# Performance work log

Measured on AMD Instinct MI355X. Metric: run time of the kernel, lower is better.

The kernel has to match this reference:

```python
import jax, jax.numpy as jnp
import numpy as np

# Hyperparameters from init_kwargs
SMOOTHNESS = 0.5
RADIUS_RATIO = 0.1  # computed in original code but never used in the mask math
IMG_SIZE = 512
BATCH = 32


def _smooth_mask(h, w, smoothness):
    """Vectorized replacement of the original per-pixel double loop.

    mask[i,j] = smoothness                       if |i-ch|^2 + |j-cw|^2 <= 1
              = max(1, dist_norm / smoothness)   otherwise
    where dist_norm = sqrt((|i-ch|/(h/2))^2 + (|j-cw|/(w/2))^2).
    Returns [h, w] float32 (broadcasts over the channel dim).
    """
    dh = jnp.abs(jnp.arange(h, dtype=jnp.float32) - (h // 2))[:, None]  # [h,1]
    dw = jnp.abs(jnp.arange(w, dtype=jnp.float32) - (w // 2))[None, :]  # [1,w]
    center = dh * dh + dw * dw <= 1.0
    dist = jnp.sqrt((dh / (h / 2)) ** 2 + (dw / (w / 2)) ** 2)
    outer = jnp.maximum(jnp.float32(1.0), dist / smoothness)
    return jnp.where(center, jnp.float32(smoothness), outer)


def setup_inputs() -> dict:
    key = jax.random.key(0)
    kx, = jax.random.split(key, 1)
    x = jax.random.normal(kx, (BATCH, 3, IMG_SIZE, IMG_SIZE), dtype=jnp.float32)
    param = jnp.ones((3, IMG_SIZE, IMG_SIZE), dtype=jnp.float32)  # nn.Parameter init
    return {"x": x, "param": param}


def reference(x, param):
    # x: [B, C, H, W] real -> complex spectrum, centered
    f = jnp.fft.fftshift(jnp.fft.fft2(x), axes=(-2, -1))
    h, w = x.shape[-2], x.shape[-1]
    mask = _smooth_mask(h, w, SMOOTHNESS)          # [H, W]
    filt = f * mask * param                        # broadcast [3,H,W] over batch
    out = jnp.fft.ifft2(jnp.fft.ifftshift(filt, axes=(-2, -1))).real
    return out
```

## Files before the change

kernel.cpp:

```cpp
#include <hip/hip_runtime.h>
#include <math.h>

#define N 512
#define CS 514
#define S8 0.70710678118654752440f

__device__ __forceinline__ float2 cadd(float2 a, float2 b){ return make_float2(a.x+b.x, a.y+b.y); }
__device__ __forceinline__ float2 csub(float2 a, float2 b){ return make_float2(a.x-b.x, a.y-b.y); }
__device__ __forceinline__ float2 cmul(float2 a, float2 b){
    return make_float2(fmaf(a.x,b.x,-(a.y*b.y)), fmaf(a.x,b.y, a.y*b.x));
}
template<int INV> __device__ __forceinline__ float2 rot90(float2 a){
    return INV ? make_float2(-a.y, a.x) : make_float2(a.y, -a.x);
}
template<int INV> __device__ __forceinline__ float2 rotW1(float2 a){
    return INV ? make_float2(S8*(a.x-a.y), S8*(a.x+a.y))
               : make_float2(S8*(a.x+a.y), S8*(a.y-a.x));
}
template<int INV> __device__ __forceinline__ float2 rotW3(float2 a){
    return INV ? make_float2(-S8*(a.x+a.y), S8*(a.x-a.y))
               : make_float2(S8*(a.y-a.x), -S8*(a.x+a.y));
}

template<int INV>
__device__ __forceinline__ void fft8(float2 v[8]) {
    float2 t0 = cadd(v[0],v[4]), t4 = csub(v[0],v[4]);
    float2 t1 = cadd(v[1],v[5]), t5 = rotW1<INV>(csub(v[1],v[5]));
    float2 t2 = cadd(v[2],v[6]), t6 = rot90<INV>(csub(v[2],v[6]));
    float2 t3 = cadd(v[3],v[7]), t7 = rotW3<INV>(csub(v[3],v[7]));
    float2 u0 = cadd(t0,t2), u2 = csub(t0,t2);
    float2 u1 = cadd(t1,t3), u3 = rot90<INV>(csub(t1,t3));
    float2 u4 = cadd(t4,t6), u6 = csub(t4,t6);
    float2 u5 = cadd(t5,t7), u7 = rot90<INV>(csub(t5,t7));
    v[0]=cadd(u0,u1); v[4]=csub(u0,u1);
    v[2]=cadd(u2,u3); v[6]=csub(u2,u3);
    v[1]=cadd(u4,u5); v[5]=csub(u4,u5);
    v[3]=cadd(u6,u7); v[7]=csub(u6,u7);
}

__device__ __forceinline__ void apply_pow(float2 v[8], float2 w1) {
    float2 w2 = cmul(w1,w1);
    float2 w3 = cmul(w2,w1);
    float2 w4 = cmul(w2,w2);
    v[1]=cmul(v[1],w1); v[2]=cmul(v[2],w2); v[3]=cmul(v[3],w3); v[4]=cmul(v[4],w4);
    v[5]=cmul(v[5],cmul(w4,w1));
    v[6]=cmul(v[6],cmul(w4,w2));
    v[7]=cmul(v[7],cmul(w4,w3));
}

#define TWO_PI 6.28318530717958647692f

__device__ __forceinline__ void fft512_fwd(float2 v[8], int l, float2* sc) {
    int hi = l >> 3, lo = l & 7;
    fft8<0>(v);
    { float s, c; __sincosf(-TWO_PI * (1.0f/512.0f) * (float)l, &s, &c);
      apply_pow(v, make_float2(c, s)); }
#pragma unroll
    for (int q = 0; q < 8; ++q) sc[q*64 + ((hi ^ q) << 3) + lo] = v[q];
#pragma unroll
    for (int b = 0; b < 8; ++b) v[b] = sc[hi*64 + ((b ^ hi) << 3) + lo];
    fft8<0>(v);
    { float s, c; __sincosf(-TWO_PI * (1.0f/64.0f) * (float)lo, &s, &c);
      apply_pow(v, make_float2(c, s)); }
#pragma unroll
    for (int q2 = 0; q2 < 8; ++q2) sc[q2*64 + ((hi ^ q2) << 3) + (lo ^ hi)] = v[q2];
#pragma unroll
    for (int cc = 0; cc < 8; ++cc) v[cc] = sc[hi*64 + ((lo ^ hi) << 3) + (cc ^ lo)];
    fft8<0>(v);
}

__device__ __forceinline__ void fft512_inv(float2 v[8], int l, float2* sc) {
    int hi = l >> 3, lo = l & 7;
    fft8<1>(v);
#pragma unroll
    for (int cc = 0; cc < 8; ++cc) sc[hi*64 + ((lo ^ hi) << 3) + (cc ^ lo)] = v[cc];
#pragma unroll
    for (int q2 = 0; q2 < 8; ++q2) v[q2] = sc[q2*64 + ((hi ^ q2) << 3) + (lo ^ hi)];
    { float s, c; __sincosf(TWO_PI * (1.0f/64.0f) * (float)lo, &s, &c);
      apply_pow(v, make_float2(c, s)); }
    fft8<1>(v);
#pragma unroll
    for (int b = 0; b < 8; ++b) sc[hi*64 + ((b ^ hi) << 3) + lo] = v[b];
#pragma unroll
    for (int q = 0; q < 8; ++q) v[q] = sc[q*64 + ((hi ^ q) << 3) + lo];
    { float s, c; __sincosf(TWO_PI * (1.0f/512.0f) * (float)l, &s, &c);
      apply_pow(v, make_float2(c, s)); }
    fft8<1>(v);
}


__global__ __launch_bounds__(512) void k_filt(const float* __restrict__ param,
                                              float* __restrict__ filt) {
    int c = blockIdx.x >> 9;
    int vv = blockIdx.x & 511;
    int u = threadIdx.x;
    int dh = (u < 256) ? u : (512 - u);
    int dw = (vv < 256) ? vv : (512 - vv);
    int d2 = dh * dh + dw * dw;
    float m = (d2 <= 1) ? 0.5f : fmaxf(1.0f, sqrtf((float)d2) * (2.0f / 256.0f));
    int su  = (u + 256) & 511,  sv  = (vv + 256) & 511;
    int su2 = (256 - u) & 511,  sv2 = (256 - vv) & 511;
    float p  = param[((size_t)c * N + su)  * N + sv];
    float p2 = param[((size_t)c * N + su2) * N + sv2];
    const float invN2 = 1.0f / ((float)N * (float)N);
    int pos = ((vv >> 7) << 7) | ((vv & 63) << 1) | ((vv >> 6) & 1);
    filt[(((size_t)c << 9) + pos) * N + u] = m * 0.5f * (p + p2) * invN2;
}

__global__ __launch_bounds__(256) void k_row_fwd(const float* __restrict__ x,
                                                 float2* __restrict__ ws, int pairBase) {
    __shared__ float2 scr[4 * 512];
    int t = threadIdx.x;
    int l = t & 63, wv = t >> 6;
    int pr = blockIdx.x >> 7;
    int row = ((blockIdx.x & 127) << 2) + wv;
    int pair = pairBase + pr;
    const float4* xa = (const float4*)(x + ((size_t)pair * N + row) * N);
    const float4* xb = (const float4*)(x + ((size_t)(pair + 48) * N + row) * N);
    float4 a0 = xa[l], a1 = xa[64 + l];
    float4 b0 = xb[l], b1 = xb[64 + l];
    float* s = (float*)(scr + wv * 512);
    ((float4*)s)[l] = a0;       ((float4*)s)[64 + l]  = a1;
    ((float4*)s)[128 + l] = b0; ((float4*)s)[192 + l] = b1;
    float2 v[8];
#pragma unroll
    for (int a = 0; a < 8; ++a) v[a] = make_float2(s[a * 64 + l], s[512 + a * 64 + l]);
    fft512_fwd(v, l, scr + wv * 512);
    float4* o = (float4*)(ws + ((size_t)pr * N + row) * N);
#pragma unroll
    for (int j = 0; j < 4; ++j)
        o[j * 64 + l] = make_float4(v[2*j].x, v[2*j].y, v[2*j+1].x, v[2*j+1].y);
}

__global__ __launch_bounds__(512) void k_col(float2* __restrict__ ws,
                                             const float* __restrict__ filt, int pairBase) {
    __shared__ float2 tile[8 * CS];
    int t = threadIdx.x;
    int l = t & 63, wv = t >> 6;
    int pr = blockIdx.x >> 6;
    int colBase = (blockIdx.x & 63) << 3;
    float2* wsImg = ws + (size_t)pr * (size_t)(N * N);

#pragma unroll
    for (int k = 0; k < 4; ++k) {
        int lin = (k << 10) + (t << 1);
        int r = lin >> 3, c = lin & 7;
        float4 f = *(const float4*)(&wsImg[(size_t)r * N + colBase + c]);
        tile[c * CS + r]       = make_float2(f.x, f.y);
        tile[(c + 1) * CS + r] = make_float2(f.z, f.w);
    }
    __syncthreads();

    float2* sc = tile + wv * CS;
    float2 v[8];
#pragma unroll
    for (int a = 0; a < 8; ++a) v[a] = sc[a * 64 + l];

    fft512_fwd(v, l, sc);

    int ch = (pairBase + pr) % 3;
    int col = colBase + wv;
    const float* fcol = filt + (((size_t)ch << 9) + col) * N;
#pragma unroll
    for (int r = 0; r < 8; ++r) {
        float f = fcol[r * 64 + l];
        v[r].x *= f; v[r].y *= f;
    }

    fft512_inv(v, l, sc);

#pragma unroll
    for (int a = 0; a < 8; ++a) sc[a * 64 + l] = v[a];
    __syncthreads();

#pragma unroll
    for (int k = 0; k < 4; ++k) {
        int lin = (k << 10) + (t << 1);
        int r = lin >> 3, c = lin & 7;
        float2 e0 = tile[c * CS + r], e1 = tile[(c + 1) * CS + r];
        *(float4*)(&wsImg[(size_t)r * N + colBase + c]) = make_float4(e0.x, e0.y, e1.x, e1.y);
    }
}

__global__ __launch_bounds__(256) void k_row_inv(const float2* __restrict__ ws,
                                                 float* __restrict__ out, int pairBase) {
    __shared__ float2 scr[4 * 512];
    int t = threadIdx.x;
    int l = t & 63, wv = t >> 6;
    int pr = blockIdx.x >> 7;
    int row = ((blockIdx.x & 127) << 2) + wv;
    int pair = pairBase + pr;
    const float4* i4 = (const float4*)(ws + ((size_t)pr * N + row) * N);
    float2 v[8];
#pragma unroll
    for (int j = 0; j < 4; ++j) {
        float4 f = i4[j * 64 + l];
        v[2*j]   = make_float2(f.x, f.y);
        v[2*j+1] = make_float2(f.z, f.w);
    }
    fft512_inv(v, l, scr + wv * 512);
    float* s = (float*)(scr + wv * 512);
#pragma unroll
    for (int a = 0; a < 8; ++a) { s[a*64 + l] = v[a].x; s[512 + a*64 + l] = v[a].y; }
    float4* oa = (float4*)(out + ((size_t)pair * N + row) * N);
    float4* ob = (float4*)(out + ((size_t)(pair + 48) * N + row) * N);
    oa[l]      = ((float4*)s)[l];
    oa[64 + l] = ((float4*)s)[64 + l];
    ob[l]      = ((float4*)s)[128 + l];
    ob[64 + l] = ((float4*)s)[192 + l];
}

extern "C" void kernel_launch(void* const* d_in, const int* in_sizes, int n_in,
                              void* d_out, int out_size, void* d_ws, size_t ws_size,
                              hipStream_t stream) {
    const float* x = (const float*)d_in[0];
    const float* param = (const float*)d_in[1];
    float* out = (float*)d_out;

    float* filt = (float*)d_ws;
    const size_t filtElems = (size_t)3 * N * N;
    float2* ws = (float2*)((char*)d_ws + filtElems * sizeof(float));

    const int NP = 48;
    size_t perImg = (size_t)N * N * sizeof(float2);
    size_t avail = (ws_size > filtElems * sizeof(float)) ? ws_size - filtElems * sizeof(float) : 0;
    int G = (int)(avail / perImg);
    if (G < 1) G = 1;
    if (G > NP) G = NP;

    k_filt<<<dim3(3 * N), dim3(N), 0, stream>>>(param, filt);

    for (int base = 0; base < NP; base += G) {
        int g = NP - base;
        if (g > G) g = G;
        k_row_fwd<<<dim3(g * 128), dim3(256), 0, stream>>>(x, ws, base);
        k_col<<<dim3(g * 64), dim3(512), 0, stream>>>(ws, filt, base);
        k_row_inv<<<dim3(g * 128), dim3(256), 0, stream>>>(ws, out, base);
    }
}
```

Before: 271.6 us.

## Process 8 rows per wave with register prefetch in row FFT kernels

The row forward and inverse FFT kernels now give each wave 8 consecutive rows. Each wave prefetches the next row's global data into registers while it computes the current row's FFT, and the grid shrinks by 8x. The column kernel is reordered so all global loads are issued before the LDS writes, and all LDS reads happen before the global stores, which batches memory operations. This is meant to hide global memory latency and cut block launch overhead. In exchange it uses more registers and leaves far fewer blocks to fill the GPU, especially when G is small.

```diff
diff --git a/kernel.cpp b/kernel.cpp
--- a/kernel.cpp
+++ b/kernel.cpp
@@ -112,24 +112,40 @@
     __shared__ float2 scr[4 * 512];
     int t = threadIdx.x;
     int l = t & 63, wv = t >> 6;
-    int pr = blockIdx.x >> 7;
-    int row = ((blockIdx.x & 127) << 2) + wv;
+    int pr = blockIdx.x >> 4;
+    int rb = blockIdx.x & 15;
+    int row0 = (rb << 5) + (wv << 3);
     int pair = pairBase + pr;
-    const float4* xa = (const float4*)(x + ((size_t)pair * N + row) * N);
-    const float4* xb = (const float4*)(x + ((size_t)(pair + 48) * N + row) * N);
-    float4 a0 = xa[l], a1 = xa[64 + l];
-    float4 b0 = xb[l], b1 = xb[64 + l];
+    const float* xaB = x + ((size_t)pair * N + row0) * N;
+    const float* xbB = x + ((size_t)(pair + 48) * N + row0) * N;
+    float2* oB = ws + ((size_t)pr * N + row0) * N;
+
     float* s = (float*)(scr + wv * 512);
-    ((float4*)s)[l] = a0;       ((float4*)s)[64 + l]  = a1;
-    ((float4*)s)[128 + l] = b0; ((float4*)s)[192 + l] = b1;
     float2 v[8];
-#pragma unroll
-    for (int a = 0; a < 8; ++a) v[a] = make_float2(s[a * 64 + l], s[512 + a * 64 + l]);
-    fft512_fwd(v, l, scr + wv * 512);
-    float4* o = (float4*)(ws + ((size_t)pr * N + row) * N);
-#pragma unroll
-    for (int j = 0; j < 4; ++j)
-        o[j * 64 + l] = make_float4(v[2*j].x, v[2*j].y, v[2*j+1].x, v[2*j+1].y);
+    float4 cA0, cA1, cB0, cB1, nA0, nA1, nB0, nB1;
+
+    cA0 = ((const float4*)xaB)[l];      cA1 = ((const float4*)xaB)[64 + l];
+    cB0 = ((const float4*)xbB)[l];      cB1 = ((const float4*)xbB)[64 + l];
+
+#pragma unroll 1
+    for (int i = 0; i < 8; ++i) {
+        if (i < 7) {
+            const float4* xa1 = (const float4*)(xaB + (size_t)(i + 1) * N);
+            const float4* xb1 = (const float4*)(xbB + (size_t)(i + 1) * N);
+            nA0 = xa1[l]; nA1 = xa1[64 + l];
+            nB0 = xb1[l]; nB1 = xb1[64 + l];
+        }
+        ((float4*)s)[l] = cA0;       ((float4*)s)[64 + l]  = cA1;
+        ((float4*)s)[128 + l] = cB0; ((float4*)s)[192 + l] = cB1;
+#pragma unroll
+        for (int a = 0; a < 8; ++a) v[a] = make_float2(s[a * 64 + l], s[512 + a * 64 + l]);
+        fft512_fwd(v, l, scr + wv * 512);
+        float4* o = (float4*)(oB + (size_t)i * N);
+#pragma unroll
+        for (int j = 0; j < 4; ++j)
+            o[j * 64 + l] = make_float4(v[2*j].x, v[2*j].y, v[2*j+1].x, v[2*j+1].y);
+        cA0 = nA0; cA1 = nA1; cB0 = nB0; cB1 = nB1;
+    }
 }
 
 __global__ __launch_bounds__(512) void k_col(float2* __restrict__ ws,
@@ -141,13 +157,19 @@
     int colBase = (blockIdx.x & 63) << 3;
     float2* wsImg = ws + (size_t)pr * (size_t)(N * N);
 
-#pragma unroll
-    for (int k = 0; k < 4; ++k) {
-        int lin = (k << 10) + (t << 1);
-        int r = lin >> 3, c = lin & 7;
-        float4 f = *(const float4*)(&wsImg[(size_t)r * N + colBase + c]);
-        tile[c * CS + r]       = make_float2(f.x, f.y);
-        tile[(c + 1) * CS + r] = make_float2(f.z, f.w);
+    float4 g[4];
+#pragma unroll
+    for (int k = 0; k < 4; ++k) {
+        int lin = (k << 10) + (t << 1);
+        int r = lin >> 3, c = lin & 7;
+        g[k] = *(const float4*)(&wsImg[(size_t)r * N + colBase + c]);
+    }
+#pragma unroll
+    for (int k = 0; k < 4; ++k) {
+        int lin = (k << 10) + (t << 1);
+        int r = lin >> 3, c = lin & 7;
+        tile[c * CS + r]       = make_float2(g[k].x, g[k].y);
+        tile[(c + 1) * CS + r] = make_float2(g[k].z, g[k].w);
     }
     __syncthreads();
 
@@ -178,7 +200,13 @@
         int lin = (k << 10) + (t << 1);
         int r = lin >> 3, c = lin & 7;
         float2 e0 = tile[c * CS + r], e1 = tile[(c + 1) * CS + r];
-        *(float4*)(&wsImg[(size_t)r * N + colBase + c]) = make_float4(e0.x, e0.y, e1.x, e1.y);
+        g[k] = make_float4(e0.x, e0.y, e1.x, e1.y);
+    }
+#pragma unroll
+    for (int k = 0; k < 4; ++k) {
+        int lin = (k << 10) + (t << 1);
+        int r = lin >> 3, c = lin & 7;
+        *(float4*)(&wsImg[(size_t)r * N + colBase + c]) = g[k];
     }
 }
 
@@ -187,27 +215,46 @@
     __shared__ float2 scr[4 * 512];
     int t = threadIdx.x;
     int l = t & 63, wv = t >> 6;
-    int pr = blockIdx.x >> 7;
-    int row = ((blockIdx.x & 127) << 2) + wv;
+    int pr = blockIdx.x >> 4;
+    int rb = blockIdx.x & 15;
+    int row0 = (rb << 5) + (wv << 3);
     int pair = pairBase + pr;
-    const float4* i4 = (const float4*)(ws + ((size_t)pr * N + row) * N);
+    const float2* iB = ws + ((size_t)pr * N + row0) * N;
+    float* oaB = out + ((size_t)pair * N + row0) * N;
+    float* obB = out + ((size_t)(pair + 48) * N + row0) * N;
+
+    float* s = (float*)(scr + wv * 512);
     float2 v[8];
-#pragma unroll
-    for (int j = 0; j < 4; ++j) {
-        float4 f = i4[j * 64 + l];
-        v[2*j]   = make_float2(f.x, f.y);
-        v[2*j+1] = make_float2(f.z, f.w);
-    }
-    fft512_inv(v, l, scr + wv * 512);
-    float* s = (float*)(scr + wv * 512);
-#pragma unroll
-    for (int a = 0; a < 8; ++a) { s[a*64 + l] = v[a].x; s[512 + a*64 + l] = v[a].y; }
-    float4* oa = (float4*)(out + ((size_t)pair * N + row) * N);
-    float4* ob = (float4*)(out + ((size_t)(pair + 48) * N + row) * N);
-    oa[l]      = ((float4*)s)[l];
-    oa[64 + l] = ((float4*)s)[64 + l];
-    ob[l]      = ((float4*)s)[128 + l];
-    ob[64 + l] = ((float4*)s)[192 + l];
+    float4 c0, c1, c2, c3, n0, n1, n2, n3;
+
+    {
+        const float4* i4 = (const float4*)iB;
+        c0 = i4[l]; c1 = i4[64 + l]; c2 = i4[128 + l]; c3 = i4[192 + l];
+    }
+
+#pragma unroll 1
+    for (int i = 0; i < 8; ++i) {
+        if (i < 7) {
+            const float4* i4 = (const float4*)(iB + (size_t)(i + 1) * N);
+            n0 = i4[l]; n1 = i4[64 + l]; n2 = i4[128 + l]; n3 = i4[192 + l];
+        }
+        v[0]=make_float2(c0.x,c0.y); v[1]=make_float2(c0.z,c0.w);
+        v[2]=make_float2(c1.x,c1.y); v[3]=make_float2(c1.z,c1.w);
+        v[4]=make_float2(c2.x,c2.y); v[5]=make_float2(c2.z,c2.w);
+        v[6]=make_float2(c3.x,c3.y); v[7]=make_float2(c3.z,c3.w);
+        fft512_inv(v, l, scr + wv * 512);
+#pragma unroll
+        for (int a = 0; a < 8; ++a) { s[a*64 + l] = v[a].x; s[512 + a*64 + l] = v[a].y; }
+        {
+            float4* oa = (float4*)(oaB + (size_t)i * N);
+            float4* ob = (float4*)(obB + (size_t)i * N);
+            oa[l]      = ((float4*)s)[l];
+            oa[64 + l] = ((float4*)s)[64 + l];
+            ob[l]      = ((float4*)s)[128 + l];
+            ob[64 + l] = ((float4*)s)[192 + l];
+        }
+        c0 = n0; c1 = n1; c2 = n2; c3 = n3;
+    }
 }
 
 extern "C" void kernel_launch(void* const* d_in, const int* in_sizes, int n_in,
@@ -233,8 +280,8 @@
     for (int base = 0; base < NP; base += G) {
         int g = NP - base;
         if (g > G) g = G;
-        k_row_fwd<<<dim3(g * 128), dim3(256), 0, stream>>>(x, ws, base);
+        k_row_fwd<<<dim3(g * 16), dim3(256), 0, stream>>>(x, ws, base);
         k_col<<<dim3(g * 64), dim3(512), 0, stream>>>(ws, filt, base);
-        k_row_inv<<<dim3(g * 128), dim3(256), 0, stream>>>(ws, out, base);
-    }
-}
+        k_row_inv<<<dim3(g * 16), dim3(256), 0, stream>>>(ws, out, base);
+    }
+}
```

After: 278.8 us. 1.03x slower.

## Fuse filter, row and column FFT passes into one cooperative persistent kernel

Applied to the files above, without the earlier changes.

Replaces the separate filter, forward-row, column and inverse-row launches with a single cooperative kernel. It is sized to the occupancy-limited block count and uses grid-wide syncs between phases. This is meant to cut launch overhead and inter-kernel gaps. It also batches the global loads and stores in the column pass ahead of the shared-memory writes. In exchange, 512-thread blocks now do the row work, grid.sync costs are added, and if the cooperative launch fails the code falls back to the old multi-kernel path.

```diff
diff --git a/kernel.cpp b/kernel.cpp
--- a/kernel.cpp
+++ b/kernel.cpp
@@ -1,8 +1,12 @@
 #include <hip/hip_runtime.h>
+#include <hip/hip_cooperative_groups.h>
 #include <math.h>
+
+namespace cg = cooperative_groups;
 
 #define N 512
 #define CS 514
+#define NP 48
 #define S8 0.70710678118654752440f
 
 __device__ __forceinline__ float2 cadd(float2 a, float2 b){ return make_float2(a.x+b.x, a.y+b.y); }
@@ -89,11 +93,11 @@
 }
 
 
-__global__ __launch_bounds__(512) void k_filt(const float* __restrict__ param,
-                                              float* __restrict__ filt) {
-    int c = blockIdx.x >> 9;
-    int vv = blockIdx.x & 511;
-    int u = threadIdx.x;
+
+__device__ __forceinline__ void filt_body(const float* __restrict__ param,
+                                          float* __restrict__ filt, int T, int u) {
+    int c = T >> 9;
+    int vv = T & 511;
     int dh = (u < 256) ? u : (512 - u);
     int dw = (vv < 256) ? vv : (512 - vv);
     int d2 = dh * dh + dw * dw;
@@ -107,6 +111,139 @@
     filt[(((size_t)c << 9) + pos) * N + u] = m * 0.5f * (p + p2) * invN2;
 }
 
+__device__ __forceinline__ void row_fwd_body(const float* __restrict__ x,
+        float2* __restrict__ ws, int pairBase, int pr, int row, int l, float2* myscr) {
+    const float* xa = x + ((size_t)(pairBase + pr) * N + row) * N;
+    const float* xb = x + ((size_t)(pairBase + pr + NP) * N + row) * N;
+    float4 a0 = ((const float4*)xa)[l], a1 = ((const float4*)xa)[64 + l];
+    float4 b0 = ((const float4*)xb)[l], b1 = ((const float4*)xb)[64 + l];
+    float* s = (float*)myscr;
+    ((float4*)s)[l] = a0;       ((float4*)s)[64 + l]  = a1;
+    ((float4*)s)[128 + l] = b0; ((float4*)s)[192 + l] = b1;
+    float2 v[8];
+#pragma unroll
+    for (int a = 0; a < 8; ++a) v[a] = make_float2(s[a * 64 + l], s[512 + a * 64 + l]);
+    fft512_fwd(v, l, myscr);
+    float4* o = (float4*)(ws + ((size_t)pr * N + row) * N);
+#pragma unroll
+    for (int j = 0; j < 4; ++j)
+        o[j * 64 + l] = make_float4(v[2*j].x, v[2*j].y, v[2*j+1].x, v[2*j+1].y);
+}
+
+__device__ __forceinline__ void row_inv_body(const float2* __restrict__ ws,
+        float* __restrict__ out, int pairBase, int pr, int row, int l, float2* myscr) {
+    const float4* i4 = (const float4*)(ws + ((size_t)pr * N + row) * N);
+    float4 f0 = i4[l], f1 = i4[64 + l], f2 = i4[128 + l], f3 = i4[192 + l];
+    float2 v[8];
+    v[0]=make_float2(f0.x,f0.y); v[1]=make_float2(f0.z,f0.w);
+    v[2]=make_float2(f1.x,f1.y); v[3]=make_float2(f1.z,f1.w);
+    v[4]=make_float2(f2.x,f2.y); v[5]=make_float2(f2.z,f2.w);
+    v[6]=make_float2(f3.x,f3.y); v[7]=make_float2(f3.z,f3.w);
+    fft512_inv(v, l, myscr);
+    float* s = (float*)myscr;
+#pragma unroll
+    for (int a = 0; a < 8; ++a) { s[a*64 + l] = v[a].x; s[512 + a*64 + l] = v[a].y; }
+    float4* oa = (float4*)(out + ((size_t)(pairBase + pr) * N + row) * N);
+    float4* ob = (float4*)(out + ((size_t)(pairBase + pr + NP) * N + row) * N);
+    oa[l]      = ((float4*)s)[l];
+    oa[64 + l] = ((float4*)s)[64 + l];
+    ob[l]      = ((float4*)s)[128 + l];
+    ob[64 + l] = ((float4*)s)[192 + l];
+}
+
+__global__ __launch_bounds__(512) void k_fused(const float* __restrict__ x,
+        const float* __restrict__ param, float* __restrict__ out,
+        float2* __restrict__ ws, float* __restrict__ filt,
+        int pairBase, int G, int doFilt)
+{
+    __shared__ float2 smem[8 * CS];
+    cg::grid_group grid = cg::this_grid();
+    int t = threadIdx.x;
+    int l = t & 63, wv = t >> 6;
+    float2* myscr = smem + wv * 512;
+
+    if (doFilt) {
+        for (int T = blockIdx.x; T < 3 * N; T += gridDim.x)
+            filt_body(param, filt, T, t);
+    }
+    int rowTasks = G << 6;
+    for (int T = blockIdx.x; T < rowTasks; T += gridDim.x)
+        row_fwd_body(x, ws, pairBase, T >> 6, ((T & 63) << 3) + wv, l, myscr);
+
+    __threadfence();
+    grid.sync();
+
+    for (int T = blockIdx.x; T < rowTasks; T += gridDim.x) {
+        int pr = T >> 6;
+        int colBase = (T & 63) << 3;
+        float2* wsImg = ws + (size_t)pr * (size_t)(N * N);
+        __syncthreads();
+
+        float4 g4[4];
+#pragma unroll
+        for (int k = 0; k < 4; ++k) {
+            int lin = (k << 10) + (t << 1);
+            int r = lin >> 3, c = lin & 7;
+            g4[k] = *(const float4*)(&wsImg[(size_t)r * N + colBase + c]);
+        }
+#pragma unroll
+        for (int k = 0; k < 4; ++k) {
+            int lin = (k << 10) + (t << 1);
+            int r = lin >> 3, c = lin & 7;
+            smem[c * CS + r]       = make_float2(g4[k].x, g4[k].y);
+            smem[(c + 1) * CS + r] = make_float2(g4[k].z, g4[k].w);
+        }
+        __syncthreads();
+
+        float2* sc = smem + wv * CS;
+        float2 v[8];
+#pragma unroll
+        for (int a = 0; a < 8; ++a) v[a] = sc[a * 64 + l];
+
+        fft512_fwd(v, l, sc);
+
+        int ch = (pairBase + pr) % 3;
+        int col = colBase + wv;
+        const float* fcol = filt + (((size_t)ch << 9) + col) * N;
+#pragma unroll
+        for (int r = 0; r < 8; ++r) {
+            float f = fcol[r * 64 + l];
+            v[r].x *= f; v[r].y *= f;
+        }
+
+        fft512_inv(v, l, sc);
+
+#pragma unroll
+        for (int a = 0; a < 8; ++a) sc[a * 64 + l] = v[a];
+        __syncthreads();
+
+#pragma unroll
+        for (int k = 0; k < 4; ++k) {
+            int lin = (k << 10) + (t << 1);
+            int r = lin >> 3, c = lin & 7;
+            float2 e0 = smem[c * CS + r], e1 = smem[(c + 1) * CS + r];
+            g4[k] = make_float4(e0.x, e0.y, e1.x, e1.y);
+        }
+#pragma unroll
+        for (int k = 0; k < 4; ++k) {
+            int lin = (k << 10) + (t << 1);
+            int r = lin >> 3, c = lin & 7;
+            *(float4*)(&wsImg[(size_t)r * N + colBase + c]) = g4[k];
+        }
+    }
+
+    __threadfence();
+    grid.sync();
+
+    for (int T = blockIdx.x; T < rowTasks; T += gridDim.x)
+        row_inv_body(ws, out, pairBase, T >> 6, ((T & 63) << 3) + wv, l, myscr);
+}
+
+__global__ __launch_bounds__(512) void k_filt(const float* __restrict__ param,
+                                              float* __restrict__ filt) {
+    filt_body(param, filt, blockIdx.x, threadIdx.x);
+}
+
 __global__ __launch_bounds__(256) void k_row_fwd(const float* __restrict__ x,
                                                  float2* __restrict__ ws, int pairBase) {
     __shared__ float2 scr[4 * 512];
@@ -114,22 +251,7 @@
     int l = t & 63, wv = t >> 6;
     int pr = blockIdx.x >> 7;
     int row = ((blockIdx.x & 127) << 2) + wv;
-    int pair = pairBase + pr;
-    const float4* xa = (const float4*)(x + ((size_t)pair * N + row) * N);
-    const float4* xb = (const float4*)(x + ((size_t)(pair + 48) * N + row) * N);
-    float4 a0 = xa[l], a1 = xa[64 + l];
-    float4 b0 = xb[l], b1 = xb[64 + l];
-    float* s = (float*)(scr + wv * 512);
-    ((float4*)s)[l] = a0;       ((float4*)s)[64 + l]  = a1;
-    ((float4*)s)[128 + l] = b0; ((float4*)s)[192 + l] = b1;
-    float2 v[8];
-#pragma unroll
-    for (int a = 0; a < 8; ++a) v[a] = make_float2(s[a * 64 + l], s[512 + a * 64 + l]);
-    fft512_fwd(v, l, scr + wv * 512);
-    float4* o = (float4*)(ws + ((size_t)pr * N + row) * N);
-#pragma unroll
-    for (int j = 0; j < 4; ++j)
-        o[j * 64 + l] = make_float4(v[2*j].x, v[2*j].y, v[2*j+1].x, v[2*j+1].y);
+    row_fwd_body(x, ws, pairBase, pr, row, l, scr + wv * 512);
 }
 
 __global__ __launch_bounds__(512) void k_col(float2* __restrict__ ws,
@@ -141,13 +263,19 @@
     int colBase = (blockIdx.x & 63) << 3;
     float2* wsImg = ws + (size_t)pr * (size_t)(N * N);
 
+    float4 g4[4];
 #pragma unroll
     for (int k = 0; k < 4; ++k) {
         int lin = (k << 10) + (t << 1);
         int r = lin >> 3, c = lin & 7;
-        float4 f = *(const float4*)(&wsImg[(size_t)r * N + colBase + c]);
-        tile[c * CS + r]       = make_float2(f.x, f.y);
-        tile[(c + 1) * CS + r] = make_float2(f.z, f.w);
+        g4[k] = *(const float4*)(&wsImg[(size_t)r * N + colBase + c]);
+    }
+#pragma unroll
+    for (int k = 0; k < 4; ++k) {
+        int lin = (k << 10) + (t << 1);
+        int r = lin >> 3, c = lin & 7;
+        tile[c * CS + r]       = make_float2(g4[k].x, g4[k].y);
+        tile[(c + 1) * CS + r] = make_float2(g4[k].z, g4[k].w);
     }
     __syncthreads();
 
@@ -155,7 +283,6 @@
     float2 v[8];
 #pragma unroll
     for (int a = 0; a < 8; ++a) v[a] = sc[a * 64 + l];
-
     fft512_fwd(v, l, sc);
 
     int ch = (pairBase + pr) % 3;
@@ -166,7 +293,6 @@
         float f = fcol[r * 64 + l];
         v[r].x *= f; v[r].y *= f;
     }
-
     fft512_inv(v, l, sc);
 
 #pragma unroll
@@ -178,7 +304,13 @@
         int lin = (k << 10) + (t << 1);
         int r = lin >> 3, c = lin & 7;
         float2 e0 = tile[c * CS + r], e1 = tile[(c + 1) * CS + r];
-        *(float4*)(&wsImg[(size_t)r * N + colBase + c]) = make_float4(e0.x, e0.y, e1.x, e1.y);
+        g4[k] = make_float4(e0.x, e0.y, e1.x, e1.y);
+    }
+#pragma unroll
+    for (int k = 0; k < 4; ++k) {
+        int lin = (k << 10) + (t << 1);
+        int r = lin >> 3, c = lin & 7;
+        *(float4*)(&wsImg[(size_t)r * N + colBase + c]) = g4[k];
     }
 }
 
@@ -189,25 +321,7 @@
     int l = t & 63, wv = t >> 6;
     int pr = blockIdx.x >> 7;
     int row = ((blockIdx.x & 127) << 2) + wv;
-    int pair = pairBase + pr;
-    const float4* i4 = (const float4*)(ws + ((size_t)pr * N + row) * N);
-    float2 v[8];
-#pragma unroll
-    for (int j = 0; j < 4; ++j) {
-        float4 f = i4[j * 64 + l];
-        v[2*j]   = make_float2(f.x, f.y);
-        v[2*j+1] = make_float2(f.z, f.w);
-    }
-    fft512_inv(v, l, scr + wv * 512);
-    float* s = (float*)(scr + wv * 512);
-#pragma unroll
-    for (int a = 0; a < 8; ++a) { s[a*64 + l] = v[a].x; s[512 + a*64 + l] = v[a].y; }
-    float4* oa = (float4*)(out + ((size_t)pair * N + row) * N);
-    float4* ob = (float4*)(out + ((size_t)(pair + 48) * N + row) * N);
-    oa[l]      = ((float4*)s)[l];
-    oa[64 + l] = ((float4*)s)[64 + l];
-    ob[l]      = ((float4*)s)[128 + l];
-    ob[64 + l] = ((float4*)s)[192 + l];
+    row_inv_body(ws, out, pairBase, pr, row, l, scr + wv * 512);
 }
 
 extern "C" void kernel_launch(void* const* d_in, const int* in_sizes, int n_in,
@@ -221,20 +335,51 @@
     const size_t filtElems = (size_t)3 * N * N;
     float2* ws = (float2*)((char*)d_ws + filtElems * sizeof(float));
 
-    const int NP = 48;
     size_t perImg = (size_t)N * N * sizeof(float2);
     size_t avail = (ws_size > filtElems * sizeof(float)) ? ws_size - filtElems * sizeof(float) : 0;
     int G = (int)(avail / perImg);
     if (G < 1) G = 1;
     if (G > NP) G = NP;
 
-    k_filt<<<dim3(3 * N), dim3(N), 0, stream>>>(param, filt);
-
-    for (int base = 0; base < NP; base += G) {
+    static int nblk = 0;
+    if (nblk == 0) {
+        int perCU = 0;
+        if (hipOccupancyMaxActiveBlocksPerMultiprocessor(&perCU, k_fused, 512, 0) != hipSuccess
+            || perCU < 1) perCU = 1;
+        int cus = 256;
+        int dev = 0;
+        hipDeviceProp_t prop;
+        if (hipGetDevice(&dev) == hipSuccess &&
+            hipGetDeviceProperties(&prop, dev) == hipSuccess &&
+            prop.multiProcessorCount > 0)
+            cus = prop.multiProcessorCount;
+        long total = (long)perCU * (long)cus;
+        if (total > 3072) total = 3072;
+        if (total < 1) total = 1;
+        nblk = (int)total;
+    }
+
+    bool coopOK = true;
+    for (int base = 0; base < NP && coopOK; base += G) {
         int g = NP - base;
         if (g > G) g = G;
-        k_row_fwd<<<dim3(g * 128), dim3(256), 0, stream>>>(x, ws, base);
-        k_col<<<dim3(g * 64), dim3(512), 0, stream>>>(ws, filt, base);
-        k_row_inv<<<dim3(g * 128), dim3(256), 0, stream>>>(ws, out, base);
-    }
-}
+        int doFilt = (base == 0) ? 1 : 0;
+        void* args[] = { (void*)&x, (void*)&param, (void*)&out,
+                         (void*)&ws, (void*)&filt, (void*)&base, (void*)&g, (void*)&doFilt };
+        hipError_t err = hipLaunchCooperativeKernel((const void*)k_fused,
+                                                    dim3(nblk), dim3(512),
+                                                    args, 0, stream);
+        if (err != hipSuccess) { coopOK = false; break; }
+    }
+
+    if (!coopOK) {
+        k_filt<<<dim3(3 * N), dim3(N), 0, stream>>>(param, filt);
+        for (int base = 0; base < NP; base += G) {
+            int g = NP - base;
+            if (g > G) g = G;
+            k_row_fwd<<<dim3(g * 128), dim3(256), 0, stream>>>(x, ws, base);
+            k_col<<<dim3(g * 64), dim3(512), 0, stream>>>(ws, filt, base);
+            k_row_inv<<<dim3(g * 128), dim3(256), 0, stream>>>(ws, out, base);
+        }
+    }
+}
```

New measurement: 486.2 us. 79.0% more time.
